# Kernel optimization log

Hardware: AMD Instinct MI355X
Metric: run time of the kernel (lower is better)

The kernel has to match this reference:

```python
import jax, jax.numpy as jnp
import numpy as np

V = 32000   # vocab_size
E = 400     # EMBEDDING_SIZE
H = 1150    # HIDDEN_SIZE
B = 16      # batch
T = 128     # seq len

# Reference corresponds to model.eval(): LockedDropout and WeightDrop (DropConnect)
# are identity at eval time, so the math is a plain 3-layer LSTM stack with tied
# embedding/output weights. PyTorch LSTM gate order: i, f, g, o.

def _lstm_layer(x_seq, W_ih, W_hh, b_ih, b_hh, hidden):
    # x_seq: (T, B, I); W_ih: (4H', I); W_hh: (4H', H'); biases: (4H',)
    pre = jnp.einsum('tbi,gi->tbg', x_seq, W_ih) + (b_ih + b_hh)  # (T,B,4H')
    h0 = jnp.zeros((x_seq.shape[1], hidden), x_seq.dtype)
    c0 = jnp.zeros_like(h0)

    def step(carry, pre_t):
        h, c = carry
        gates = pre_t + h @ W_hh.T               # (B, 4H')
        i, f, g, o = jnp.split(gates, 4, axis=-1)
        i = jax.nn.sigmoid(i); f = jax.nn.sigmoid(f)
        g = jnp.tanh(g);       o = jax.nn.sigmoid(o)
        c = f * c + i * g
        h = o * jnp.tanh(c)
        return (h, c), h

    (h_T, c_T), ys = jax.lax.scan(step, (h0, c0), pre)
    return ys, h_T, c_T  # ys: (T,B,H')


def setup_inputs() -> dict:
    key = jax.random.key(0)
    ks = jax.random.split(key, 16)
    s = 1.0 / np.sqrt(H)
    u = lambda k, shape: jax.random.uniform(k, shape, jnp.float32, -s, s)
    inp = {
        'emb':   jax.random.uniform(ks[0], (V, E), jnp.float32, -0.1, 0.1),
        'W_ih1': u(ks[1], (4 * H, E)),  'W_hh1': u(ks[2], (4 * H, H)),
        'b_ih1': u(ks[3], (4 * H,)),    'b_hh1': u(ks[4], (4 * H,)),
        'W_ih2': u(ks[5], (4 * H, H)),  'W_hh2': u(ks[6], (4 * H, H)),
        'b_ih2': u(ks[7], (4 * H,)),    'b_hh2': u(ks[8], (4 * H,)),
        'W_ih3': u(ks[9], (4 * E, H)),  'W_hh3': u(ks[10], (4 * E, E)),
        'b_ih3': u(ks[11], (4 * E,)),   'b_hh3': u(ks[12], (4 * E,)),
        'lin_b': u(ks[13], (V,)),
        'x': jax.random.randint(ks[14], (B, T), 0, V, jnp.int32),
    }
    return inp


def reference(emb, W_ih1, W_hh1, b_ih1, b_hh1,
              W_ih2, W_hh2, b_ih2, b_hh2,
              W_ih3, W_hh3, b_ih3, b_hh3,
              lin_b, x):
    xe = emb[x]                       # (B,T,E)
    xs = jnp.transpose(xe, (1, 0, 2)) # (T,B,E)
    xs, h1, c1 = _lstm_layer(xs, W_ih1, W_hh1, b_ih1, b_hh1, H)
    xs, h2, c2 = _lstm_layer(xs, W_ih2, W_hh2, b_ih2, b_hh2, H)
    xs, h3, c3 = _lstm_layer(xs, W_ih3, W_hh3, b_ih3, b_hh3, E)
    xb = jnp.transpose(xs, (1, 0, 2))                 # (B,T,E)
    logits = jnp.einsum('bte,ve->btv', xb, emb) + lin_b  # tied weights
    out = jnp.transpose(logits, (0, 2, 1))            # (B,V,T)
    return out, h1, h2, h3, c1, c2, c3
```

## Files before the change

kernel.cpp:

```cpp
#include <hip/hip_runtime.h>

typedef _Float16 f16;
typedef _Float16 f16x8 __attribute__((ext_vector_type(8)));
typedef float f32x4 __attribute__((ext_vector_type(4)));

#define BB 16
#define TT 128
#define VV 32000
#define EE 400
#define HH 1150
#define MM 2048

#define NWG1 72
#define NWG2 144
#define NWG3 26
#define NWGT (NWG1+NWG2+NWG3)
#define NSTEPS 130

__device__ __forceinline__ float sigm(float x){ return 1.f/(1.f + __expf(-x)); }
__device__ __forceinline__ float ftanh(float x){ return 2.f/(1.f + __expf(-2.f*x)) - 1.f; }

__device__ __forceinline__ void ld16c(f16x8& d, const f16* p){
    asm volatile("global_load_dwordx4 %0, %1, off sc0 sc1"
                 : "=v"(d) : "v"(p) : "memory");
}
__device__ __forceinline__ void st2c(f16* p, f16 v){
    asm volatile("global_store_short %0, %1, off sc0 sc1"
                 :: "v"(p), "v"(v) : "memory");
}


__global__ void conv_emb(const float* __restrict__ src, f16* __restrict__ dst){
    int v = blockIdx.y;
    int k = blockIdx.x*256 + threadIdx.x;
    if (k >= 416) return;
    float val = (k < EE) ? src[v*EE + k] : 0.f;
    dst[v*416 + k] = (f16)val;
}

__global__ void embed_gather(const float* __restrict__ emb, const int* __restrict__ x,
                             f16* __restrict__ dst){
    int m = blockIdx.y;
    int k = blockIdx.x*256 + threadIdx.x;
    if (k >= 416) return;
    int t = m >> 4, b = m & 15;
    int row = x[b*TT + t];
    float val = (k < EE) ? emb[row*EE + k] : 0.f;
    dst[m*416 + k] = (f16)val;
}

__global__ void conv_w(const float* __restrict__ src, f16* __restrict__ dst,
                       int Hout, int Ksrc, int Kp){
    int n = blockIdx.y;
    int k = blockIdx.x*256 + threadIdx.x;
    if (k >= Kp) return;
    int j = n >> 2, g = n & 3;
    float val = (j < Hout && k < Ksrc) ? src[(g*Hout + j)*Ksrc + k] : 0.f;
    dst[(size_t)n*Kp + k] = (f16)val;
}

__global__ void conv_bias(const float* __restrict__ bi, const float* __restrict__ bh,
                          float* __restrict__ dst, int Hout, int Np){
    int n = blockIdx.x*256 + threadIdx.x;
    if (n >= Np) return;
    int j = n >> 2, g = n & 3;
    dst[n] = (j < Hout) ? (bi[g*Hout + j] + bh[g*Hout + j]) : 0.f;
}

template<int SC>
__global__ __launch_bounds__(256) void gemm16(
    const f16* __restrict__ A, const f16* __restrict__ B,
    const float* __restrict__ bias, float* __restrict__ C,
    int Kp, int Nst)
{
    __shared__ __align__(16) f16 lA[128*32];
    __shared__ __align__(16) f16 lB[128*32];
    const int lane = threadIdx.x & 63;
    const int wid  = threadIdx.x >> 6;
    const int m0 = blockIdx.y * 128, n0 = blockIdx.x * 128;
    f32x4 acc[4][4] = {};
    const int sr = threadIdx.x >> 2;
    const int sc = (threadIdx.x & 3) * 8;
    for (int k0 = 0; k0 < Kp; k0 += 32) {
        __syncthreads();
        *(f16x8*)&lA[ sr      *32 + sc] = *(const f16x8*)&A[(size_t)(m0 + sr     )*Kp + k0 + sc];
        *(f16x8*)&lA[(sr + 64)*32 + sc] = *(const f16x8*)&A[(size_t)(m0 + sr + 64)*Kp + k0 + sc];
        *(f16x8*)&lB[ sr      *32 + sc] = *(const f16x8*)&B[(size_t)(n0 + sr     )*Kp + k0 + sc];
        *(f16x8*)&lB[(sr + 64)*32 + sc] = *(const f16x8*)&B[(size_t)(n0 + sr + 64)*Kp + k0 + sc];
        __syncthreads();
        const int wr = (wid >> 1) * 64, wc = (wid & 1) * 64;
        f16x8 af[4], bf[4];
        #pragma unroll
        for (int i = 0; i < 4; ++i)
            af[i] = *(const f16x8*)&lA[(wr + i*16 + (lane & 15))*32 + (lane >> 4)*8];
        #pragma unroll
        for (int j = 0; j < 4; ++j)
            bf[j] = *(const f16x8*)&lB[(wc + j*16 + (lane & 15))*32 + (lane >> 4)*8];
        #pragma unroll
        for (int i = 0; i < 4; ++i)
            #pragma unroll
            for (int j = 0; j < 4; ++j)
                acc[i][j] = __builtin_amdgcn_mfma_f32_16x16x32_f16(af[i], bf[j], acc[i][j], 0, 0, 0);
    }
    const int wr = (wid >> 1) * 64, wc = (wid & 1) * 64;
    #pragma unroll
    for (int i = 0; i < 4; ++i) {
        #pragma unroll
        for (int j = 0; j < 4; ++j) {
            int gc = n0 + wc + j*16 + (lane & 15);
            float bb = bias[gc];
            #pragma unroll
            for (int r = 0; r < 4; ++r) {
                int gr = m0 + wr + i*16 + (lane >> 4)*4 + r;
                float v = acc[i][j][r] + bb;
                if (SC) C[((size_t)(gr >> 7)*VV + gc)*TT + (gr & 127)] = v;
                else    C[(size_t)gr*Nst + gc] = v;
            }
        }
    }
}


template<int KIH, int KHH, int DELAY, int NG>
__device__ __forceinline__ void lstm_role(
    float (&red)[4][16][66], float (&cst)[16][16],
    const float* __restrict__ pre,
    const float* __restrict__ bias,
    const f16* __restrict__ Wih,
    const f16* __restrict__ Whh,
    const f16* __restrict__ xA, const f16* __restrict__ xB,
    f16* __restrict__ hA, f16* __restrict__ hB,
    f16* __restrict__ xs3,
    float* __restrict__ hout, float* __restrict__ cout,
    unsigned* __restrict__ arrive, int bid, int H)
{
    constexpr int HpHH = KHH * 128;
    constexpr int KIHA = (KIH > 0) ? KIH : 1;
    constexpr int G = NG * 16;
    const int lane = threadIdx.x & 63, kw = threadIdx.x >> 6;
    const int n0 = bid * G;
    const int nwg = gridDim.x;
    cst[threadIdx.x & 15][threadIdx.x >> 4] = 0.f;
    const int arow = lane & 15, aoff = (lane >> 4) * 8;
    const size_t hofsHH = (size_t)arow * HpHH + kw * (KHH * 32) + aoff;
    const size_t hofsIH = (size_t)arow * 1152 + kw * 288 + aoff;

    f16x8 wh[NG][KHH];
    #pragma unroll
    for (int g = 0; g < NG; ++g) {
        const f16* wp = Whh + (size_t)(n0 + g*16 + arow) * HpHH + kw * (KHH*32) + aoff;
        #pragma unroll
        for (int i = 0; i < KHH; ++i) wh[g][i] = *(const f16x8*)(wp + i*32);
    }
    f16x8 wi[NG][KIHA];
    if constexpr (KIH > 0) {
        #pragma unroll
        for (int g = 0; g < NG; ++g) {
            const f16* wp = Wih + (size_t)(n0 + g*16 + arow) * 1152 + kw * 288 + aoff;
            #pragma unroll
            for (int i = 0; i < KIH; ++i) wi[g][i] = *(const f16x8*)(wp + i*32);
        }
    }
    const int b  = threadIdx.x & 15;
    const int jl = threadIdx.x >> 4;
    f32x4 bias4 = {0.f,0.f,0.f,0.f};
    if constexpr (KIH > 0) {
        if (threadIdx.x < NG*64) bias4 = *(const f32x4*)(bias + n0 + jl*4);
    }
    __syncthreads();

    for (int s = 0; s < NSTEPS; ++s) {
        const int t = s - DELAY;
        if (t >= 0 && t < TT) {
            const f16* hp = ((t & 1) ? hB : hA) + hofsHH;
            f16* hw       =  (t & 1) ? hA : hB;
            f32x4 p4;
            if constexpr (KIH == 0) {
                if (threadIdx.x < NG*64)
                    p4 = *(const f32x4*)(pre + (size_t)(t*16 + b)*4608 + n0 + jl*4);
            }
            f16x8 xv[KIHA], hv[KHH];
            if constexpr (KIH > 0) {
                const f16* xp = ((t & 1) ? xA : xB) + hofsIH;
                #pragma unroll
                for (int i = 0; i < KIH; ++i) ld16c(xv[i], xp + i*32);
            }
            #pragma unroll
            for (int i = 0; i < KHH; ++i) ld16c(hv[i], hp + i*32);
            asm volatile("s_waitcnt vmcnt(0)" ::: "memory");
            __builtin_amdgcn_sched_barrier(0);

            f32x4 acc[NG] = {};
            if constexpr (KIH > 0) {
                #pragma unroll
                for (int i = 0; i < KIH; ++i)
                    #pragma unroll
                    for (int g = 0; g < NG; ++g)
                        acc[g] = __builtin_amdgcn_mfma_f32_16x16x32_f16(xv[i], wi[g][i], acc[g], 0, 0, 0);
            }
            #pragma unroll
            for (int i = 0; i < KHH; ++i)
                #pragma unroll
                for (int g = 0; g < NG; ++g)
                    acc[g] = __builtin_amdgcn_mfma_f32_16x16x32_f16(hv[i], wh[g][i], acc[g], 0, 0, 0);

            #pragma unroll
            for (int g = 0; g < NG; ++g)
                #pragma unroll
                for (int r = 0; r < 4; ++r)
                    red[kw][(lane >> 4)*4 + r][g*16 + (lane & 15)] = acc[g][r];
            __syncthreads();
            if (threadIdx.x < NG*64) {
                const int nb = jl * 4;
                f32x4 base = (KIH > 0) ? bias4 : p4;
                float gi = base[0] + red[0][b][nb+0] + red[1][b][nb+0] + red[2][b][nb+0] + red[3][b][nb+0];
                float gf = base[1] + red[0][b][nb+1] + red[1][b][nb+1] + red[2][b][nb+1] + red[3][b][nb+1];
                float gg = base[2] + red[0][b][nb+2] + red[1][b][nb+2] + red[2][b][nb+2] + red[3][b][nb+2];
                float go = base[3] + red[0][b][nb+3] + red[1][b][nb+3] + red[2][b][nb+3] + red[3][b][nb+3];
                float c = sigm(gf) * cst[b][jl] + sigm(gi) * ftanh(gg);
                float h = sigm(go) * ftanh(c);
                cst[b][jl] = c;
                const int j = (n0 >> 2) + jl;
                st2c(hw + b*HpHH + j, (f16)h);
                if constexpr (DELAY == 2) xs3[(size_t)(b*TT + t)*416 + j] = (f16)h;
                if (t == TT-1 && j < H) { hout[b*H + j] = h; cout[b*H + j] = c; }
                asm volatile("s_waitcnt vmcnt(0)" ::: "memory");
            }
        }
        if (s == NSTEPS-1) break;
        __syncthreads();
        if (threadIdx.x == 0)
            __hip_atomic_store(&arrive[blockIdx.x * 16], (unsigned)(s + 1),
                               __ATOMIC_RELAXED, __HIP_MEMORY_SCOPE_AGENT);
        for (int w = threadIdx.x; w < nwg; w += 256) {
            while (__hip_atomic_load(&arrive[w * 16], __ATOMIC_RELAXED,
                                     __HIP_MEMORY_SCOPE_AGENT) < (unsigned)(s + 1))
                __builtin_amdgcn_s_sleep(1);
        }
        __syncthreads();
    }
}

__global__ __launch_bounds__(256, 1) void lstm_mega(
    const float* __restrict__ pre1,
    const float* __restrict__ bias2, const float* __restrict__ bias3,
    const f16* __restrict__ whh1,
    const f16* __restrict__ wih2, const f16* __restrict__ whh2,
    const f16* __restrict__ wih3, const f16* __restrict__ whh3,
    f16* h1A, f16* h1B, f16* h2A, f16* h2B, f16* h3A, f16* h3B,
    f16* xs3,
    float* h1o, float* c1o, float* h2o, float* c2o, float* h3o, float* c3o,
    unsigned* arrive)
{
    __shared__ float red[4][16][66];
    __shared__ float cst[16][16];
    const int bx = blockIdx.x;
    if (bx < NWG1) {
        lstm_role<0,9,0,4>(red, cst, pre1, nullptr, nullptr, whh1,
                           nullptr, nullptr, h1A, h1B, nullptr,
                           h1o, c1o, arrive, bx, HH);
    } else if (bx < NWG1 + NWG2) {
        lstm_role<9,9,1,2>(red, cst, nullptr, bias2, wih2, whh2,
                           h1A, h1B, h2A, h2B, nullptr,
                           h2o, c2o, arrive, bx - NWG1, HH);
    } else {
        lstm_role<9,4,2,4>(red, cst, nullptr, bias3, wih3, whh3,
                           h2A, h2B, h3A, h3B, xs3,
                           h3o, c3o, arrive, bx - NWG1 - NWG2, EE);
    }
}

extern "C" void kernel_launch(void* const* d_in, const int* in_sizes, int n_in,
                              void* d_out, int out_size, void* d_ws, size_t ws_size,
                              hipStream_t stream)
{
    const float* emb  = (const float*)d_in[0];
    const float* Wih1 = (const float*)d_in[1];
    const float* Whh1 = (const float*)d_in[2];
    const float* bih1 = (const float*)d_in[3];
    const float* bhh1 = (const float*)d_in[4];
    const float* Wih2 = (const float*)d_in[5];
    const float* Whh2 = (const float*)d_in[6];
    const float* bih2 = (const float*)d_in[7];
    const float* bhh2 = (const float*)d_in[8];
    const float* Wih3 = (const float*)d_in[9];
    const float* Whh3 = (const float*)d_in[10];
    const float* bih3 = (const float*)d_in[11];
    const float* bhh3 = (const float*)d_in[12];
    const float* linb = (const float*)d_in[13];
    const int*   x    = (const int*)d_in[14];
    float* out = (float*)d_out;
    char*  ws  = (char*)d_ws;
    char*  outc = (char*)d_out;

    const size_t ARR  = 0;
    const size_t H1A  = 21760;
    const size_t H1B  = H1A + 36864;
    const size_t H2A  = H1B + 36864;
    const size_t H2B  = H2A + 36864;
    const size_t H3A  = H2B + 36864;
    const size_t H3B  = H3A + 16384;
    const size_t ZEND = H3B + 16384;
    size_t off = ZEND;
    auto alloc = [&](size_t bytes){ size_t r = off; off += (bytes + 255) & ~(size_t)255; return r; };
    const size_t EMBBF = alloc((size_t)VV*416*2);
    const size_t XS0   = alloc((size_t)MM*416*2);
    const size_t XS3   = alloc((size_t)MM*416*2);
    const size_t WIH1  = alloc((size_t)4608*416*2);
    const size_t B1    = alloc((size_t)4608*4);
    const size_t B2    = alloc((size_t)4608*4);
    const size_t B3    = alloc((size_t)1664*4);

    f16* emb_bf = (f16*)(ws + EMBBF);
    f16* xs0    = (f16*)(ws + XS0);
    f16* xs3    = (f16*)(ws + XS3);
    f16* wih1p  = (f16*)(ws + WIH1);
    float* bias1 = (float*)(ws + B1);
    float* bias2 = (float*)(ws + B2);
    float* bias3 = (float*)(ws + B3);
    unsigned* arr = (unsigned*)(ws + ARR);

    float* pre1 = out;
    const size_t OW_HH1 = 37748736;
    const size_t OW_IH2 = OW_HH1 + 10616832;
    const size_t OW_HH2 = OW_IH2 + 10616832;
    const size_t OW_IH3 = OW_HH2 + 10616832;
    const size_t OW_HH3 = OW_IH3 + 3833856;
    f16* whh1p = (f16*)(outc + OW_HH1);
    f16* wih2p = (f16*)(outc + OW_IH2);
    f16* whh2p = (f16*)(outc + OW_HH2);
    f16* wih3p = (f16*)(outc + OW_IH3);
    f16* whh3p = (f16*)(outc + OW_HH3);

    float* H1O = out + 65536000;  float* H2O = H1O + 18400;  float* H3O = H2O + 18400;
    float* C1O = H3O + 6400;      float* C2O = C1O + 18400;  float* C3O = C2O + 18400;

    hipMemsetAsync(d_ws, 0, ZEND, stream);

    conv_emb    <<<dim3(2, VV), 256, 0, stream>>>(emb, emb_bf);
    embed_gather<<<dim3(2, MM), 256, 0, stream>>>(emb, x, xs0);

    conv_w   <<<dim3(2, 4608), 256, 0, stream>>>(Wih1, wih1p, HH, EE, 416);
    conv_bias<<<dim3(18),      256, 0, stream>>>(bih1, bhh1, bias1, HH, 4608);
    gemm16<0><<<dim3(36, 16),  256, 0, stream>>>(xs0, wih1p, bias1, pre1, 416, 4608);

    conv_w   <<<dim3(5, 4608), 256, 0, stream>>>(Whh1, whh1p, HH, HH, 1152);
    conv_w   <<<dim3(5, 4608), 256, 0, stream>>>(Wih2, wih2p, HH, HH, 1152);
    conv_w   <<<dim3(5, 4608), 256, 0, stream>>>(Whh2, whh2p, HH, HH, 1152);
    conv_w   <<<dim3(5, 1664), 256, 0, stream>>>(Wih3, wih3p, EE, HH, 1152);
    conv_w   <<<dim3(2, 1664), 256, 0, stream>>>(Whh3, whh3p, EE, EE, 512);
    conv_bias<<<dim3(18),      256, 0, stream>>>(bih2, bhh2, bias2, HH, 4608);
    conv_bias<<<dim3(7),       256, 0, stream>>>(bih3, bhh3, bias3, EE, 1664);

    lstm_mega<<<dim3(NWGT), 256, 0, stream>>>(
        pre1, bias2, bias3, whh1p, wih2p, whh2p, wih3p, whh3p,
        (f16*)(ws+H1A), (f16*)(ws+H1B), (f16*)(ws+H2A), (f16*)(ws+H2B),
        (f16*)(ws+H3A), (f16*)(ws+H3B),
        xs3, H1O, C1O, H2O, C2O, H3O, C3O, arr);

    gemm16<1><<<dim3(250, 16), 256, 0, stream>>>(xs3, emb_bf, linb, out, 416, 0);
}
```

Measured before the change: 1.196 ms.

## Replace global all-block barrier with per-layer step counters and full h history

The lockstep grid-wide barrier across all three LSTM layers, with its fixed skew, is replaced by per-timestep arrival counters for each layer. Each layer waits only on its own previous step and on the producer layer's matching step, so layers can run in a wavefront that is not pinned to one global step. Hidden states are now stored as a full time-indexed history in spare output memory instead of ping-pong buffers, which removes write-after-read hazards between layers. The cost is more memory traffic and plain (non-coherent-flagged) loads of h, which rely on the relaxed atomics and cache behaviour to make the new values visible.

```diff
diff --git a/kernel.cpp b/kernel.cpp
--- a/kernel.cpp
+++ b/kernel.cpp
@@ -15,15 +15,10 @@
 #define NWG2 144
 #define NWG3 26
 #define NWGT (NWG1+NWG2+NWG3)
-#define NSTEPS 130
 
 __device__ __forceinline__ float sigm(float x){ return 1.f/(1.f + __expf(-x)); }
 __device__ __forceinline__ float ftanh(float x){ return 2.f/(1.f + __expf(-2.f*x)) - 1.f; }
 
-__device__ __forceinline__ void ld16c(f16x8& d, const f16* p){
-    asm volatile("global_load_dwordx4 %0, %1, off sc0 sc1"
-                 : "=v"(d) : "v"(p) : "memory");
-}
 __device__ __forceinline__ void st2c(f16* p, f16 v){
     asm volatile("global_store_short %0, %1, off sc0 sc1"
                  :: "v"(p), "v"(v) : "memory");
@@ -121,25 +116,27 @@
 }
 
 
-template<int KIH, int KHH, int DELAY, int NG>
+template<int KIH, int KHH, int NG>
 __device__ __forceinline__ void lstm_role(
     float (&red)[4][16][66], float (&cst)[16][16],
     const float* __restrict__ pre,
     const float* __restrict__ bias,
     const f16* __restrict__ Wih,
     const f16* __restrict__ Whh,
-    const f16* __restrict__ xA, const f16* __restrict__ xB,
-    f16* __restrict__ hA, f16* __restrict__ hB,
+    const f16* __restrict__ xseq,
+    f16* __restrict__ hseq,
     f16* __restrict__ xs3,
     float* __restrict__ hout, float* __restrict__ cout,
-    unsigned* __restrict__ arrive, int bid, int H)
+    const unsigned* __restrict__ cprod, unsigned* __restrict__ cown,
+    int nprod, int nown, int bid, int H, int l3)
 {
     constexpr int HpHH = KHH * 128;
+    constexpr int SLO  = 16 * HpHH;
+    constexpr int SLP  = 16 * 1152;
     constexpr int KIHA = (KIH > 0) ? KIH : 1;
     constexpr int G = NG * 16;
     const int lane = threadIdx.x & 63, kw = threadIdx.x >> 6;
     const int n0 = bid * G;
-    const int nwg = gridDim.x;
     cst[threadIdx.x & 15][threadIdx.x >> 4] = 0.f;
     const int arow = lane & 15, aoff = (lane >> 4) * 8;
     const size_t hofsHH = (size_t)arow * HpHH + kw * (KHH * 32) + aoff;
@@ -169,75 +166,77 @@
     }
     __syncthreads();
 
-    for (int s = 0; s < NSTEPS; ++s) {
-        const int t = s - DELAY;
-        if (t >= 0 && t < TT) {
-            const f16* hp = ((t & 1) ? hB : hA) + hofsHH;
-            f16* hw       =  (t & 1) ? hA : hB;
-            f32x4 p4;
-            if constexpr (KIH == 0) {
-                if (threadIdx.x < NG*64)
-                    p4 = *(const f32x4*)(pre + (size_t)(t*16 + b)*4608 + n0 + jl*4);
+    for (int t = 0; t < TT; ++t) {
+        f32x4 p4;
+        if constexpr (KIH == 0) {
+            if (threadIdx.x < NG*64)
+                p4 = *(const f32x4*)(pre + (size_t)(t*16 + b)*4608 + n0 + jl*4);
+        }
+        if (threadIdx.x == 0) {
+            if constexpr (KIH > 0) {
+                while (__hip_atomic_load((unsigned*)cprod + (size_t)(t+1)*16,
+                                         __ATOMIC_RELAXED, __HIP_MEMORY_SCOPE_AGENT) < (unsigned)nprod)
+                    __builtin_amdgcn_s_sleep(1);
             }
-            f16x8 xv[KIHA], hv[KHH];
-            if constexpr (KIH > 0) {
-                const f16* xp = ((t & 1) ? xA : xB) + hofsIH;
-                #pragma unroll
-                for (int i = 0; i < KIH; ++i) ld16c(xv[i], xp + i*32);
+            if (t > 0) {
+                while (__hip_atomic_load(cown + (size_t)t*16,
+                                         __ATOMIC_RELAXED, __HIP_MEMORY_SCOPE_AGENT) < (unsigned)nown)
+                    __builtin_amdgcn_s_sleep(1);
             }
-            #pragma unroll
-            for (int i = 0; i < KHH; ++i) ld16c(hv[i], hp + i*32);
-            asm volatile("s_waitcnt vmcnt(0)" ::: "memory");
-            __builtin_amdgcn_sched_barrier(0);
-
-            f32x4 acc[NG] = {};
-            if constexpr (KIH > 0) {
-                #pragma unroll
-                for (int i = 0; i < KIH; ++i)
-                    #pragma unroll
-                    for (int g = 0; g < NG; ++g)
-                        acc[g] = __builtin_amdgcn_mfma_f32_16x16x32_f16(xv[i], wi[g][i], acc[g], 0, 0, 0);
-            }
-            #pragma unroll
-            for (int i = 0; i < KHH; ++i)
+        }
+        __syncthreads();
+        __builtin_amdgcn_sched_barrier(0);
+
+        f16x8 xv[KIHA], hv[KHH];
+        if constexpr (KIH > 0) {
+            const f16* xp = xseq + (size_t)(t+1)*SLP + hofsIH;
+            #pragma unroll
+            for (int i = 0; i < KIH; ++i) xv[i] = *(const f16x8*)(xp + i*32);
+        }
+        const f16* hp = hseq + (size_t)t*SLO + hofsHH;
+        #pragma unroll
+        for (int i = 0; i < KHH; ++i) hv[i] = *(const f16x8*)(hp + i*32);
+
+        f32x4 acc[NG] = {};
+        if constexpr (KIH > 0) {
+            #pragma unroll
+            for (int i = 0; i < KIH; ++i)
                 #pragma unroll
                 for (int g = 0; g < NG; ++g)
-                    acc[g] = __builtin_amdgcn_mfma_f32_16x16x32_f16(hv[i], wh[g][i], acc[g], 0, 0, 0);
-
+                    acc[g] = __builtin_amdgcn_mfma_f32_16x16x32_f16(xv[i], wi[g][i], acc[g], 0, 0, 0);
+        }
+        #pragma unroll
+        for (int i = 0; i < KHH; ++i)
             #pragma unroll
             for (int g = 0; g < NG; ++g)
-                #pragma unroll
-                for (int r = 0; r < 4; ++r)
-                    red[kw][(lane >> 4)*4 + r][g*16 + (lane & 15)] = acc[g][r];
-            __syncthreads();
-            if (threadIdx.x < NG*64) {
-                const int nb = jl * 4;
-                f32x4 base = (KIH > 0) ? bias4 : p4;
-                float gi = base[0] + red[0][b][nb+0] + red[1][b][nb+0] + red[2][b][nb+0] + red[3][b][nb+0];
-                float gf = base[1] + red[0][b][nb+1] + red[1][b][nb+1] + red[2][b][nb+1] + red[3][b][nb+1];
-                float gg = base[2] + red[0][b][nb+2] + red[1][b][nb+2] + red[2][b][nb+2] + red[3][b][nb+2];
-                float go = base[3] + red[0][b][nb+3] + red[1][b][nb+3] + red[2][b][nb+3] + red[3][b][nb+3];
-                float c = sigm(gf) * cst[b][jl] + sigm(gi) * ftanh(gg);
-                float h = sigm(go) * ftanh(c);
-                cst[b][jl] = c;
-                const int j = (n0 >> 2) + jl;
-                st2c(hw + b*HpHH + j, (f16)h);
-                if constexpr (DELAY == 2) xs3[(size_t)(b*TT + t)*416 + j] = (f16)h;
-                if (t == TT-1 && j < H) { hout[b*H + j] = h; cout[b*H + j] = c; }
-                asm volatile("s_waitcnt vmcnt(0)" ::: "memory");
-            }
-        }
-        if (s == NSTEPS-1) break;
+                acc[g] = __builtin_amdgcn_mfma_f32_16x16x32_f16(hv[i], wh[g][i], acc[g], 0, 0, 0);
+
+        #pragma unroll
+        for (int g = 0; g < NG; ++g)
+            #pragma unroll
+            for (int r = 0; r < 4; ++r)
+                red[kw][(lane >> 4)*4 + r][g*16 + (lane & 15)] = acc[g][r];
+        __syncthreads();
+        if (threadIdx.x < NG*64) {
+            const int nb = jl * 4;
+            f32x4 base = (KIH > 0) ? bias4 : p4;
+            float gi = base[0] + red[0][b][nb+0] + red[1][b][nb+0] + red[2][b][nb+0] + red[3][b][nb+0];
+            float gf = base[1] + red[0][b][nb+1] + red[1][b][nb+1] + red[2][b][nb+1] + red[3][b][nb+1];
+            float gg = base[2] + red[0][b][nb+2] + red[1][b][nb+2] + red[2][b][nb+2] + red[3][b][nb+2];
+            float go = base[3] + red[0][b][nb+3] + red[1][b][nb+3] + red[2][b][nb+3] + red[3][b][nb+3];
+            float c = sigm(gf) * cst[b][jl] + sigm(gi) * ftanh(gg);
+            float h = sigm(go) * ftanh(c);
+            cst[b][jl] = c;
+            const int j = (n0 >> 2) + jl;
+            st2c(hseq + (size_t)(t+1)*SLO + b*HpHH + j, (f16)h);
+            if (l3) xs3[(size_t)(b*TT + t)*416 + j] = (f16)h;
+            if (t == TT-1 && j < H) { hout[b*H + j] = h; cout[b*H + j] = c; }
+            asm volatile("s_waitcnt vmcnt(0)" ::: "memory");
+        }
         __syncthreads();
         if (threadIdx.x == 0)
-            __hip_atomic_store(&arrive[blockIdx.x * 16], (unsigned)(s + 1),
-                               __ATOMIC_RELAXED, __HIP_MEMORY_SCOPE_AGENT);
-        for (int w = threadIdx.x; w < nwg; w += 256) {
-            while (__hip_atomic_load(&arrive[w * 16], __ATOMIC_RELAXED,
-                                     __HIP_MEMORY_SCOPE_AGENT) < (unsigned)(s + 1))
-                __builtin_amdgcn_s_sleep(1);
-        }
-        __syncthreads();
+            __hip_atomic_fetch_add(cown + (size_t)(t+1)*16, 1u,
+                                   __ATOMIC_RELAXED, __HIP_MEMORY_SCOPE_AGENT);
     }
 }
 
@@ -247,26 +246,26 @@
     const f16* __restrict__ whh1,
     const f16* __restrict__ wih2, const f16* __restrict__ whh2,
     const f16* __restrict__ wih3, const f16* __restrict__ whh3,
-    f16* h1A, f16* h1B, f16* h2A, f16* h2B, f16* h3A, f16* h3B,
+    f16* hs1, f16* hs2, f16* hs3,
     f16* xs3,
     float* h1o, float* c1o, float* h2o, float* c2o, float* h3o, float* c3o,
-    unsigned* arrive)
+    unsigned* cnt1, unsigned* cnt2, unsigned* cnt3)
 {
     __shared__ float red[4][16][66];
     __shared__ float cst[16][16];
     const int bx = blockIdx.x;
     if (bx < NWG1) {
-        lstm_role<0,9,0,4>(red, cst, pre1, nullptr, nullptr, whh1,
-                           nullptr, nullptr, h1A, h1B, nullptr,
-                           h1o, c1o, arrive, bx, HH);
+        lstm_role<0,9,4>(red, cst, pre1, nullptr, nullptr, whh1,
+                         nullptr, hs1, nullptr, h1o, c1o,
+                         nullptr, cnt1, 0, NWG1, bx, HH, 0);
     } else if (bx < NWG1 + NWG2) {
-        lstm_role<9,9,1,2>(red, cst, nullptr, bias2, wih2, whh2,
-                           h1A, h1B, h2A, h2B, nullptr,
-                           h2o, c2o, arrive, bx - NWG1, HH);
+        lstm_role<9,9,2>(red, cst, nullptr, bias2, wih2, whh2,
+                         hs1, hs2, nullptr, h2o, c2o,
+                         cnt1, cnt2, NWG1, NWG2, bx - NWG1, HH, 0);
     } else {
-        lstm_role<9,4,2,4>(red, cst, nullptr, bias3, wih3, whh3,
-                           h2A, h2B, h3A, h3B, xs3,
-                           h3o, c3o, arrive, bx - NWG1 - NWG2, EE);
+        lstm_role<9,4,4>(red, cst, nullptr, bias3, wih3, whh3,
+                         hs2, hs3, xs3, h3o, c3o,
+                         cnt2, cnt3, NWG2, NWG3, bx - NWG1 - NWG2, EE, 1);
     }
 }
 
@@ -293,14 +292,8 @@
     char*  ws  = (char*)d_ws;
     char*  outc = (char*)d_out;
 
-    const size_t ARR  = 0;
-    const size_t H1A  = 21760;
-    const size_t H1B  = H1A + 36864;
-    const size_t H2A  = H1B + 36864;
-    const size_t H2B  = H2A + 36864;
-    const size_t H3A  = H2B + 36864;
-    const size_t H3B  = H3A + 16384;
-    const size_t ZEND = H3B + 16384;
+    const size_t CNT1 = 0, CNT2 = 8320, CNT3 = 16640;
+    const size_t ZEND = 25088;
     size_t off = ZEND;
     auto alloc = [&](size_t bytes){ size_t r = off; off += (bytes + 255) & ~(size_t)255; return r; };
     const size_t EMBBF = alloc((size_t)VV*416*2);
@@ -318,7 +311,9 @@
     float* bias1 = (float*)(ws + B1);
     float* bias2 = (float*)(ws + B2);
     float* bias3 = (float*)(ws + B3);
-    unsigned* arr = (unsigned*)(ws + ARR);
+    unsigned* cnt1 = (unsigned*)(ws + CNT1);
+    unsigned* cnt2 = (unsigned*)(ws + CNT2);
+    unsigned* cnt3 = (unsigned*)(ws + CNT3);
 
     float* pre1 = out;
     const size_t OW_HH1 = 37748736;
@@ -326,16 +321,25 @@
     const size_t OW_HH2 = OW_IH2 + 10616832;
     const size_t OW_IH3 = OW_HH2 + 10616832;
     const size_t OW_HH3 = OW_IH3 + 3833856;
+    const size_t HS1   = 75137024;
+    const size_t HS2   = HS1 + 4755456;
+    const size_t HS3   = HS2 + 4755456;
     f16* whh1p = (f16*)(outc + OW_HH1);
     f16* wih2p = (f16*)(outc + OW_IH2);
     f16* whh2p = (f16*)(outc + OW_HH2);
     f16* wih3p = (f16*)(outc + OW_IH3);
     f16* whh3p = (f16*)(outc + OW_HH3);
+    f16* hs1   = (f16*)(outc + HS1);
+    f16* hs2   = (f16*)(outc + HS2);
+    f16* hs3   = (f16*)(outc + HS3);
 
     float* H1O = out + 65536000;  float* H2O = H1O + 18400;  float* H3O = H2O + 18400;
     float* C1O = H3O + 6400;      float* C2O = C1O + 18400;  float* C3O = C2O + 18400;
 
     hipMemsetAsync(d_ws, 0, ZEND, stream);
+    hipMemsetAsync(outc + HS1, 0, 36864, stream);
+    hipMemsetAsync(outc + HS2, 0, 36864, stream);
+    hipMemsetAsync(outc + HS3, 0, 16384, stream);
 
     conv_emb    <<<dim3(2, VV), 256, 0, stream>>>(emb, emb_bf);
     embed_gather<<<dim3(2, MM), 256, 0, stream>>>(emb, x, xs0);
@@ -354,9 +358,8 @@
 
     lstm_mega<<<dim3(NWGT), 256, 0, stream>>>(
         pre1, bias2, bias3, whh1p, wih2p, whh2p, wih3p, whh3p,
-        (f16*)(ws+H1A), (f16*)(ws+H1B), (f16*)(ws+H2A), (f16*)(ws+H2B),
-        (f16*)(ws+H3A), (f16*)(ws+H3B),
-        xs3, H1O, C1O, H2O, C2O, H3O, C3O, arr);
+        hs1, hs2, hs3,
+        xs3, H1O, C1O, H2O, C2O, H3O, C3O, cnt1, cnt2, cnt3);
 
     gemm16<1><<<dim3(250, 16), 256, 0, stream>>>(xs3, emb_bf, linb, out, 416, 0);
 }
```

After: 1.309 ms. 1.1x slower.
